# Optimization experiments

Measured on AMD Instinct MI355X. Metric: run time of the kernel, lower is better.

## Reference

```python
import jax, jax.numpy as jnp
import numpy as np
from math import sqrt

D_MODEL = 768
D_T = 256
N_HEADS = 12
HEAD_DIM = D_MODEL // N_HEADS
SCALE = sqrt(HEAD_DIM)


def setup_inputs() -> dict:
    key = jax.random.key(0)
    ks = jax.random.split(key, 11)
    b, l = 8, 1024
    inv = 1.0 / sqrt(D_MODEL)
    inv_t = 1.0 / sqrt(D_T)
    return {
        "x": jax.random.normal(ks[0], (b, l, D_MODEL), dtype=jnp.float32),
        "t": jax.random.normal(ks[1], (b, D_T), dtype=jnp.float32),
        "rel_pos_bias": jax.random.normal(ks[2], (N_HEADS, l, l), dtype=jnp.float32),
        # torch Linear weights: [out_features, in_features]
        "Wx_q": jax.random.normal(ks[3], (D_MODEL, D_MODEL), dtype=jnp.float32) * inv,
        "Wx_k": jax.random.normal(ks[4], (D_MODEL, D_MODEL), dtype=jnp.float32) * inv,
        "Wx_v": jax.random.normal(ks[5], (D_MODEL, D_MODEL), dtype=jnp.float32) * inv,
        "Wt_q": jax.random.normal(ks[6], (D_MODEL, D_T), dtype=jnp.float32) * inv_t,
        "Wt_k": jax.random.normal(ks[7], (D_MODEL, D_T), dtype=jnp.float32) * inv_t,
        "Wt_v": jax.random.normal(ks[8], (D_MODEL, D_T), dtype=jnp.float32) * inv_t,
        "W_o": jax.random.normal(ks[9], (D_MODEL, D_MODEL), dtype=jnp.float32) * inv,
        "b_o": jax.random.normal(ks[10], (D_MODEL,), dtype=jnp.float32) * 0.01,
    }


def _split_heads(y):
    # [b, l, n*d] -> [b, n, l, d]
    b, l, _ = y.shape
    return y.reshape(b, l, N_HEADS, HEAD_DIM).transpose(0, 2, 1, 3)


def reference(x, t, rel_pos_bias, Wx_q, Wx_k, Wx_v, Wt_q, Wt_k, Wt_v, W_o, b_o):
    # time-conditioned QKV: per-batch additive shift broadcast over seq
    q = _split_heads(x @ Wx_q.T + (t @ Wt_q.T)[:, None, :])
    k = _split_heads(x @ Wx_k.T + (t @ Wt_k.T)[:, None, :])
    v = _split_heads(x @ Wx_v.T + (t @ Wt_v.T)[:, None, :])
    attn = jnp.einsum("bnld,bnmd->bnlm", q, k) / SCALE
    attn = attn + rel_pos_bias  # [n,l,l] broadcasts over batch
    probs = jax.nn.softmax(attn, axis=-1)
    o = jnp.einsum("bnlm,bnmd->bnld", probs, v)
    b, _, l, _ = o.shape
    o = o.transpose(0, 2, 1, 3).reshape(b, l, D_MODEL)
    return o @ W_o.T + b_o
```

## Files before the change

### kernel.cpp

```cpp
#include <hip/hip_runtime.h>
#include <hip/hip_bf16.h>
#include <stdint.h>

typedef __bf16 bf16_t;
typedef __attribute__((ext_vector_type(8))) __bf16 bf16x8;
typedef __attribute__((ext_vector_type(4))) __bf16 bf16x4;
typedef __attribute__((ext_vector_type(4))) float f32x4;

#define DEVI __device__ __forceinline__

DEVI void gll16(const void* g, void* lds_base_wave_uniform) {
  __builtin_amdgcn_global_load_lds(
      (const __attribute__((address_space(1))) uint32_t*)(uintptr_t)g,
      (__attribute__((address_space(3))) uint32_t*)(uintptr_t)lds_base_wave_uniform,
      16, 0, 0);
}

__global__ void cvt_f32_to_bf16(const float* __restrict__ src, bf16_t* __restrict__ dst, int n) {
  int i = (blockIdx.x * blockDim.x + threadIdx.x) * 4;
  if (i >= n) return;
  float4 v = *(const float4*)(src + i);
  bf16x4 o = {(bf16_t)v.x, (bf16_t)v.y, (bf16_t)v.z, (bf16_t)v.w};
  *(bf16x4*)(dst + i) = o;
}

__global__ void shift_kernel(const float* __restrict__ t,
                             const float* __restrict__ wtq,
                             const float* __restrict__ wtk,
                             const float* __restrict__ wtv,
                             float* __restrict__ shift) {
  int idx = blockIdx.x * blockDim.x + threadIdx.x;
  if (idx >= 8 * 2304) return;
  int b = idx / 2304, n = idx % 2304;
  const float* w = (n < 768) ? (wtq + (size_t)n * 256)
                 : (n < 1536) ? (wtk + (size_t)(n - 768) * 256)
                              : (wtv + (size_t)(n - 1536) * 256);
  const float4* tv = (const float4*)(t + (size_t)b * 256);
  const float4* wv = (const float4*)w;
  float acc = 0.f;
#pragma unroll 8
  for (int i = 0; i < 64; i++) {
    float4 a = tv[i], c = wv[i];
    acc += a.x * c.x + a.y * c.y + a.z * c.z + a.w * c.w;
  }
  shift[idx] = acc;
}

template <int MODE>
__global__ __launch_bounds__(256, 2) void gemm_bt(
    const bf16_t* __restrict__ A, const bf16_t* __restrict__ B,
    const float* __restrict__ add, void* __restrict__ Cout,
    int M, int N, int K) {
  __shared__ alignas(16) bf16_t As[128 * 32];
  __shared__ alignas(16) bf16_t Bs[128 * 32];
  const int t = threadIdx.x, l = t & 63, w = t >> 6;
  const int wr = w >> 1, wc = w & 1;
  const int bm = blockIdx.x, bn = blockIdx.y;

  f32x4 acc[4][4] = {};

  const int srow = t >> 2;
  const int scol = (t & 3) * 8;
  const bf16_t* Ab = A + ((size_t)bm * 128 + srow) * K + scol;
  const bf16_t* Bb = B + ((size_t)bn * 128 + srow) * K + scol;
  char* AsB = (char*)As + w * 1024;
  char* BsB = (char*)Bs + w * 1024;
  const size_t K64 = (size_t)64 * K;

  const int ro = (l & 15) * 32 + (l >> 4) * 8;
  const bf16_t* ApA = As + (wr * 64) * 32 + ro;
  const bf16_t* BpB = Bs + (wc * 64) * 32 + ro;

  for (int k0 = 0; k0 < K; k0 += 32) {
    __syncthreads();
    gll16(Ab + k0, AsB);
    gll16(Ab + K64 + k0, AsB + 4096);
    gll16(Bb + k0, BsB);
    gll16(Bb + K64 + k0, BsB + 4096);
    __syncthreads();
    bf16x8 af[4], bfr[4];
#pragma unroll
    for (int i = 0; i < 4; i++) {
      af[i]  = *(const bf16x8*)(ApA + i * 16 * 32);
      bfr[i] = *(const bf16x8*)(BpB + i * 16 * 32);
    }
#pragma unroll
    for (int mi = 0; mi < 4; mi++)
#pragma unroll
      for (int ni = 0; ni < 4; ni++)
        acc[mi][ni] = __builtin_amdgcn_mfma_f32_16x16x32_bf16(af[mi], bfr[ni], acc[mi][ni], 0, 0, 0);
  }

  const int row0 = bm * 128 + wr * 64 + (l >> 4) * 4;
  const int col0 = bn * 128 + wc * 64 + (l & 15);
  if (MODE == 0) {
    bf16_t* C = (bf16_t*)Cout;
    const float* sh = add + (size_t)((bm * 128) >> 10) * N;
#pragma unroll
    for (int ni = 0; ni < 4; ni++) {
      const int col = col0 + ni * 16;
      const float s0 = sh[col];
#pragma unroll
      for (int mi = 0; mi < 4; mi++)
#pragma unroll
        for (int i = 0; i < 4; i++)
          C[(size_t)(row0 + mi * 16 + i) * N + col] = (bf16_t)(acc[mi][ni][i] + s0);
    }
  } else {
    float* C = (float*)Cout;
#pragma unroll
    for (int ni = 0; ni < 4; ni++) {
      const int col = col0 + ni * 16;
      const float s0 = add[col];
#pragma unroll
      for (int mi = 0; mi < 4; mi++)
#pragma unroll
        for (int i = 0; i < 4; i++)
          C[(size_t)(row0 + mi * 16 + i) * N + col] = acc[mi][ni][i] + s0;
    }
  }
}

__global__ __launch_bounds__(256, 2) void attn_fused(
    const bf16_t* __restrict__ qkv,
    const float* __restrict__ bias,
    bf16_t* __restrict__ o) {
  const int id = blockIdx.x;
  const int slot = id >> 3;
  const int qt = slot & 15;
  const int grp = (id & 7) + 8 * (slot >> 4);
  const int h = grp % 12, b = grp / 12;
  const int t = threadIdx.x, l = t & 63, w = t >> 6;

  __shared__ alignas(16) bf16_t Vt[64 * 64];
  __shared__ alignas(16) bf16_t Ps[4][16 * 64];

  const size_t rowb = (size_t)b * 1024;

  bf16x8 qf[2];
  {
    const bf16_t* qp = qkv + (rowb + qt * 64 + w * 16 + (l & 15)) * 2304 + h * 64 + (l >> 4) * 8;
    qf[0] = *(const bf16x8*)qp;
    qf[1] = *(const bf16x8*)(qp + 32);
  }

  const float* bbase = bias + ((size_t)h << 20)
                     + (size_t)(qt * 64 + w * 16 + (l >> 4) * 4) * 1024 + (l & 15);
  const bf16_t* kbase = qkv + rowb * 2304 + 768 + h * 64 + (l >> 4) * 8;

  float m_run[4] = {-INFINITY, -INFINITY, -INFINITY, -INFINITY};
  float l_run[4] = {0.f, 0.f, 0.f, 0.f};
  f32x4 oacc[4] = {};

  const float LOG2E = 1.44269504088896f;
  const float C1 = 0.125f * 1.44269504088896f;

  for (int kt = 0; kt < 16; kt++) {
    bf16x8 kf[4][2];
    {
      const bf16_t* kb = kbase + (size_t)(kt * 64) * 2304;
#pragma unroll
      for (int nf = 0; nf < 4; nf++) {
        const bf16_t* kr = kb + (size_t)(nf * 16 + (l & 15)) * 2304;
        kf[nf][0] = *(const bf16x8*)kr;
        kf[nf][1] = *(const bf16x8*)(kr + 32);
      }
    }
    float barr[4][4];
    {
      const float* bb = bbase + kt * 64;
#pragma unroll
      for (int i = 0; i < 4; i++)
#pragma unroll
        for (int nf = 0; nf < 4; nf++)
          barr[i][nf] = bb[(size_t)i * 1024 + nf * 16];
    }

    __syncthreads();
    {
      const bf16_t* vp = qkv + (rowb + kt * 64 + l) * 2304 + 1536 + h * 64 + w * 16;
      bf16x8 v0 = *(const bf16x8*)vp;
      bf16x8 v1 = *(const bf16x8*)(vp + 8);
#pragma unroll
      for (int j = 0; j < 16; j++) {
        const int d = w * 16 + j;
        const int addr = d * 64 + (((l >> 3) ^ (d & 7)) * 8) + (l & 7);
        Vt[addr] = (j < 8) ? v0[j] : v1[j - 8];
      }
    }

    f32x4 sv[4];
#pragma unroll
    for (int nf = 0; nf < 4; nf++) {
      f32x4 z = {0.f, 0.f, 0.f, 0.f};
      z = __builtin_amdgcn_mfma_f32_16x16x32_bf16(qf[0], kf[nf][0], z, 0, 0, 0);
      z = __builtin_amdgcn_mfma_f32_16x16x32_bf16(qf[1], kf[nf][1], z, 0, 0, 0);
      sv[nf] = z;
    }

    float p[4][4];
    float alpha[4];
#pragma unroll
    for (int i = 0; i < 4; i++) {
      float lg[4];
#pragma unroll
      for (int nf = 0; nf < 4; nf++)
        lg[nf] = fmaf(sv[nf][i], C1, barr[i][nf] * LOG2E);
      float mx = fmaxf(fmaxf(lg[0], lg[1]), fmaxf(lg[2], lg[3]));
      mx = fmaxf(mx, __shfl_xor(mx, 1));
      mx = fmaxf(mx, __shfl_xor(mx, 2));
      mx = fmaxf(mx, __shfl_xor(mx, 4));
      mx = fmaxf(mx, __shfl_xor(mx, 8));
      const float mnew = fmaxf(m_run[i], mx);
      alpha[i] = exp2f(m_run[i] - mnew);
      m_run[i] = mnew;
      float rs = 0.f;
#pragma unroll
      for (int nf = 0; nf < 4; nf++) {
        p[nf][i] = exp2f(lg[nf] - mnew);
        rs += p[nf][i];
      }
      rs += __shfl_xor(rs, 1);
      rs += __shfl_xor(rs, 2);
      rs += __shfl_xor(rs, 4);
      rs += __shfl_xor(rs, 8);
      l_run[i] = l_run[i] * alpha[i] + rs;
    }

    bf16_t* Pw = Ps[w];
#pragma unroll
    for (int nf = 0; nf < 4; nf++)
#pragma unroll
      for (int i = 0; i < 4; i++) {
        const int rq = (l >> 4) * 4 + i;
        const int kp = nf * 16 + (l & 15);
        Pw[rq * 64 + (((kp >> 3) ^ (rq & 7)) * 8) + (kp & 7)] = (bf16_t)p[nf][i];
      }
#pragma unroll
    for (int nf2 = 0; nf2 < 4; nf2++)
#pragma unroll
      for (int i = 0; i < 4; i++)
        oacc[nf2][i] *= alpha[i];

    __syncthreads();

    bf16x8 pf[2];
#pragma unroll
    for (int kc = 0; kc < 2; kc++) {
      const int rq = l & 15;
      const int chunk = kc * 4 + (l >> 4);
      pf[kc] = *(const bf16x8*)(Pw + rq * 64 + ((chunk ^ (rq & 7)) * 8));
    }
#pragma unroll
    for (int nf2 = 0; nf2 < 4; nf2++) {
      const int d = nf2 * 16 + (l & 15);
      const bf16_t* vb = Vt + d * 64;
      bf16x8 vf0 = *(const bf16x8*)(vb + (((l >> 4) ^ (d & 7)) * 8));
      bf16x8 vf1 = *(const bf16x8*)(vb + ((((l >> 4) + 4) ^ (d & 7)) * 8));
      oacc[nf2] = __builtin_amdgcn_mfma_f32_16x16x32_bf16(pf[0], vf0, oacc[nf2], 0, 0, 0);
      oacc[nf2] = __builtin_amdgcn_mfma_f32_16x16x32_bf16(pf[1], vf1, oacc[nf2], 0, 0, 0);
    }
  }

#pragma unroll
  for (int i = 0; i < 4; i++) {
    const float inv = 1.0f / l_run[i];
    const size_t row = rowb + qt * 64 + w * 16 + (l >> 4) * 4 + i;
#pragma unroll
    for (int nf2 = 0; nf2 < 4; nf2++)
      o[row * 768 + h * 64 + nf2 * 16 + (l & 15)] = (bf16_t)(oacc[nf2][i] * inv);
  }
}

extern "C" void kernel_launch(void* const* d_in, const int* in_sizes, int n_in,
                              void* d_out, int out_size, void* d_ws, size_t ws_size,
                              hipStream_t stream) {
  const float* x    = (const float*)d_in[0];
  const float* tin  = (const float*)d_in[1];
  const float* bias = (const float*)d_in[2];
  const float* Wxq  = (const float*)d_in[3];
  const float* Wxk  = (const float*)d_in[4];
  const float* Wxv  = (const float*)d_in[5];
  const float* Wtq  = (const float*)d_in[6];
  const float* Wtk  = (const float*)d_in[7];
  const float* Wtv  = (const float*)d_in[8];
  const float* Wo   = (const float*)d_in[9];
  const float* bo   = (const float*)d_in[10];
  float* out = (float*)d_out;

  char* ws = (char*)d_ws;
  bf16_t* x_bf    = (bf16_t*)(ws);
  bf16_t* wcat    = (bf16_t*)(ws + 12582912);
  bf16_t* wo_bf   = (bf16_t*)(ws + 16121856);
  float*  shift   = (float*) (ws + 17301504);
  bf16_t* qkvb    = (bf16_t*)(ws + 17375232);
  bf16_t* obuf    = (bf16_t*)(ws + 55123968);

  const int W = 768 * 768;
  cvt_f32_to_bf16<<<6144, 256, 0, stream>>>(x, x_bf, 8192 * 768);
  cvt_f32_to_bf16<<<576, 256, 0, stream>>>(Wxq, wcat, W);
  cvt_f32_to_bf16<<<576, 256, 0, stream>>>(Wxk, wcat + W, W);
  cvt_f32_to_bf16<<<576, 256, 0, stream>>>(Wxv, wcat + 2 * W, W);
  cvt_f32_to_bf16<<<576, 256, 0, stream>>>(Wo, wo_bf, W);
  shift_kernel<<<72, 256, 0, stream>>>(tin, Wtq, Wtk, Wtv, shift);
  gemm_bt<0><<<dim3(64, 18), 256, 0, stream>>>(x_bf, wcat, shift, qkvb, 8192, 2304, 768);
  attn_fused<<<1536, 256, 0, stream>>>(qkvb, bias, obuf);
  gemm_bt<1><<<dim3(64, 6), 256, 0, stream>>>(obuf, wo_bf, bo, out, 8192, 768, 768);
}
```

Measured before the change: 344.7 us.

## Transpose QK MFMA so each lane owns one query row; lazy softmax rescale

The S=QK^T MFMA operands are swapped, so each lane holds four consecutive key columns of a single query row. This allows vectorized float4 bias loads, a row max and row sum done with only two cross-lane shuffles, and packed bf16x4 stores of P to LDS. The online-softmax rescale is skipped unless some row max grows by more than 8 in log2 units, and launch bounds are raised to 4 blocks per CU. Global V loads are issued before the barrier and P is read back before the second barrier. The risks are register pressure under the tighter occupancy bound and possible exp2 overflow headroom from deferred rescaling, though the threshold keeps values bounded.

```diff
diff --git a/kernel.cpp b/kernel.cpp
--- a/kernel.cpp
+++ b/kernel.cpp
@@ -121,7 +121,7 @@
   }
 }
 
-__global__ __launch_bounds__(256, 2) void attn_fused(
+__global__ __launch_bounds__(256, 4) void attn_fused(
     const bf16_t* __restrict__ qkv,
     const float* __restrict__ bias,
     bf16_t* __restrict__ o) {
@@ -131,132 +131,132 @@
   const int grp = (id & 7) + 8 * (slot >> 4);
   const int h = grp % 12, b = grp / 12;
   const int t = threadIdx.x, l = t & 63, w = t >> 6;
+  const int s = l & 15, g = l >> 4;
 
   __shared__ alignas(16) bf16_t Vt[64 * 64];
   __shared__ alignas(16) bf16_t Ps[4][16 * 64];
 
   const size_t rowb = (size_t)b * 1024;
+  const int qrow = qt * 64 + w * 16 + s;
 
   bf16x8 qf[2];
   {
-    const bf16_t* qp = qkv + (rowb + qt * 64 + w * 16 + (l & 15)) * 2304 + h * 64 + (l >> 4) * 8;
+    const bf16_t* qp = qkv + (rowb + qrow) * 2304 + h * 64 + g * 8;
     qf[0] = *(const bf16x8*)qp;
     qf[1] = *(const bf16x8*)(qp + 32);
   }
 
-  const float* bbase = bias + ((size_t)h << 20)
-                     + (size_t)(qt * 64 + w * 16 + (l >> 4) * 4) * 1024 + (l & 15);
-  const bf16_t* kbase = qkv + rowb * 2304 + 768 + h * 64 + (l >> 4) * 8;
-
-  float m_run[4] = {-INFINITY, -INFINITY, -INFINITY, -INFINITY};
-  float l_run[4] = {0.f, 0.f, 0.f, 0.f};
+  const bf16_t* kbase = qkv + rowb * 2304 + 768 + h * 64 + g * 8;
+  const float*  bbase = bias + ((size_t)h << 20) + (size_t)qrow * 1024 + g * 4;
+
+  float m_run = -INFINITY, l_run = 0.f;
   f32x4 oacc[4] = {};
-
   const float LOG2E = 1.44269504088896f;
   const float C1 = 0.125f * 1.44269504088896f;
 
   for (int kt = 0; kt < 16; kt++) {
     bf16x8 kf[4][2];
     {
-      const bf16_t* kb = kbase + (size_t)(kt * 64) * 2304;
+      const bf16_t* kb = kbase + (size_t)(kt * 64 + s) * 2304;
 #pragma unroll
       for (int nf = 0; nf < 4; nf++) {
-        const bf16_t* kr = kb + (size_t)(nf * 16 + (l & 15)) * 2304;
+        const bf16_t* kr = kb + (size_t)(nf * 16) * 2304;
         kf[nf][0] = *(const bf16x8*)kr;
         kf[nf][1] = *(const bf16x8*)(kr + 32);
       }
     }
-    float barr[4][4];
+    f32x4 bv[4];
     {
       const float* bb = bbase + kt * 64;
 #pragma unroll
-      for (int i = 0; i < 4; i++)
-#pragma unroll
-        for (int nf = 0; nf < 4; nf++)
-          barr[i][nf] = bb[(size_t)i * 1024 + nf * 16];
-    }
-
-    __syncthreads();
+      for (int nf = 0; nf < 4; nf++)
+        bv[nf] = *(const f32x4*)(bb + nf * 16);
+    }
+    bf16x8 v0, v1;
     {
       const bf16_t* vp = qkv + (rowb + kt * 64 + l) * 2304 + 1536 + h * 64 + w * 16;
-      bf16x8 v0 = *(const bf16x8*)vp;
-      bf16x8 v1 = *(const bf16x8*)(vp + 8);
-#pragma unroll
-      for (int j = 0; j < 16; j++) {
-        const int d = w * 16 + j;
-        const int addr = d * 64 + (((l >> 3) ^ (d & 7)) * 8) + (l & 7);
-        Vt[addr] = (j < 8) ? v0[j] : v1[j - 8];
-      }
+      v0 = *(const bf16x8*)vp;
+      v1 = *(const bf16x8*)(vp + 8);
+    }
+
+    __syncthreads();
+#pragma unroll
+    for (int j = 0; j < 16; j++) {
+      const int d = w * 16 + j;
+      const int addr = d * 64 + (((l >> 3) ^ (d & 7)) * 8) + (l & 7);
+      Vt[addr] = (j < 8) ? v0[j] : v1[j - 8];
     }
 
     f32x4 sv[4];
 #pragma unroll
     for (int nf = 0; nf < 4; nf++) {
       f32x4 z = {0.f, 0.f, 0.f, 0.f};
-      z = __builtin_amdgcn_mfma_f32_16x16x32_bf16(qf[0], kf[nf][0], z, 0, 0, 0);
-      z = __builtin_amdgcn_mfma_f32_16x16x32_bf16(qf[1], kf[nf][1], z, 0, 0, 0);
+      z = __builtin_amdgcn_mfma_f32_16x16x32_bf16(kf[nf][0], qf[0], z, 0, 0, 0);
+      z = __builtin_amdgcn_mfma_f32_16x16x32_bf16(kf[nf][1], qf[1], z, 0, 0, 0);
       sv[nf] = z;
     }
 
-    float p[4][4];
-    float alpha[4];
-#pragma unroll
-    for (int i = 0; i < 4; i++) {
-      float lg[4];
-#pragma unroll
-      for (int nf = 0; nf < 4; nf++)
-        lg[nf] = fmaf(sv[nf][i], C1, barr[i][nf] * LOG2E);
-      float mx = fmaxf(fmaxf(lg[0], lg[1]), fmaxf(lg[2], lg[3]));
-      mx = fmaxf(mx, __shfl_xor(mx, 1));
-      mx = fmaxf(mx, __shfl_xor(mx, 2));
-      mx = fmaxf(mx, __shfl_xor(mx, 4));
-      mx = fmaxf(mx, __shfl_xor(mx, 8));
-      const float mnew = fmaxf(m_run[i], mx);
-      alpha[i] = exp2f(m_run[i] - mnew);
-      m_run[i] = mnew;
-      float rs = 0.f;
+    float lg[4][4];
+#pragma unroll
+    for (int nf = 0; nf < 4; nf++)
+#pragma unroll
+      for (int i = 0; i < 4; i++)
+        lg[nf][i] = fmaf(sv[nf][i], C1, bv[nf][i] * LOG2E);
+
+    float mx = fmaxf(fmaxf(fmaxf(lg[0][0], lg[0][1]), fmaxf(lg[0][2], lg[0][3])),
+                     fmaxf(fmaxf(lg[1][0], lg[1][1]), fmaxf(lg[1][2], lg[1][3])));
+    mx = fmaxf(mx, fmaxf(fmaxf(fmaxf(lg[2][0], lg[2][1]), fmaxf(lg[2][2], lg[2][3])),
+                         fmaxf(fmaxf(lg[3][0], lg[3][1]), fmaxf(lg[3][2], lg[3][3]))));
+    mx = fmaxf(mx, __shfl_xor(mx, 16));
+    mx = fmaxf(mx, __shfl_xor(mx, 32));
+
+    if (!__all(mx - m_run <= 8.0f)) {
+      const float mnew = fmaxf(m_run, mx);
+      const float alpha = exp2f(m_run - mnew);
+      m_run = mnew;
+      l_run *= alpha;
+#pragma unroll
+      for (int i = 0; i < 4; i++) {
+        const float a_pv = __shfl(alpha, g * 4 + i);
+#pragma unroll
+        for (int nf2 = 0; nf2 < 4; nf2++) oacc[nf2][i] *= a_pv;
+      }
+    }
+
+    float rs = 0.f;
+#pragma unroll
+    for (int nf = 0; nf < 4; nf++)
+#pragma unroll
+      for (int i = 0; i < 4; i++) {
+        lg[nf][i] = exp2f(lg[nf][i] - m_run);
+        rs += lg[nf][i];
+      }
+    rs += __shfl_xor(rs, 16);
+    rs += __shfl_xor(rs, 32);
+    l_run += rs;
+
+    bf16_t* Pw = Ps[w];
+    {
+      char* pb = (char*)Pw + s * 128 + (g & 1) * 8;
 #pragma unroll
       for (int nf = 0; nf < 4; nf++) {
-        p[nf][i] = exp2f(lg[nf] - mnew);
-        rs += p[nf][i];
+        bf16x4 pk = {(bf16_t)lg[nf][0], (bf16_t)lg[nf][1], (bf16_t)lg[nf][2], (bf16_t)lg[nf][3]};
+        *(bf16x4*)(pb + ((2 * nf + (g >> 1)) ^ (s & 7)) * 16) = pk;
       }
-      rs += __shfl_xor(rs, 1);
-      rs += __shfl_xor(rs, 2);
-      rs += __shfl_xor(rs, 4);
-      rs += __shfl_xor(rs, 8);
-      l_run[i] = l_run[i] * alpha[i] + rs;
-    }
-
-    bf16_t* Pw = Ps[w];
-#pragma unroll
-    for (int nf = 0; nf < 4; nf++)
-#pragma unroll
-      for (int i = 0; i < 4; i++) {
-        const int rq = (l >> 4) * 4 + i;
-        const int kp = nf * 16 + (l & 15);
-        Pw[rq * 64 + (((kp >> 3) ^ (rq & 7)) * 8) + (kp & 7)] = (bf16_t)p[nf][i];
-      }
-#pragma unroll
-    for (int nf2 = 0; nf2 < 4; nf2++)
-#pragma unroll
-      for (int i = 0; i < 4; i++)
-        oacc[nf2][i] *= alpha[i];
+    }
+    bf16x8 pf[2];
+#pragma unroll
+    for (int c = 0; c < 2; c++)
+      pf[c] = *(const bf16x8*)((char*)Pw + s * 128 + ((4 * c + g) ^ (s & 7)) * 16);
 
     __syncthreads();
 
-    bf16x8 pf[2];
-#pragma unroll
-    for (int kc = 0; kc < 2; kc++) {
-      const int rq = l & 15;
-      const int chunk = kc * 4 + (l >> 4);
-      pf[kc] = *(const bf16x8*)(Pw + rq * 64 + ((chunk ^ (rq & 7)) * 8));
-    }
 #pragma unroll
     for (int nf2 = 0; nf2 < 4; nf2++) {
-      const int d = nf2 * 16 + (l & 15);
+      const int d = nf2 * 16 + s;
       const bf16_t* vb = Vt + d * 64;
-      bf16x8 vf0 = *(const bf16x8*)(vb + (((l >> 4) ^ (d & 7)) * 8));
-      bf16x8 vf1 = *(const bf16x8*)(vb + ((((l >> 4) + 4) ^ (d & 7)) * 8));
+      bf16x8 vf0 = *(const bf16x8*)(vb + ((g ^ (d & 7)) * 8));
+      bf16x8 vf1 = *(const bf16x8*)(vb + (((g + 4) ^ (d & 7)) * 8));
       oacc[nf2] = __builtin_amdgcn_mfma_f32_16x16x32_bf16(pf[0], vf0, oacc[nf2], 0, 0, 0);
       oacc[nf2] = __builtin_amdgcn_mfma_f32_16x16x32_bf16(pf[1], vf1, oacc[nf2], 0, 0, 0);
     }
@@ -264,11 +264,11 @@
 
 #pragma unroll
   for (int i = 0; i < 4; i++) {
-    const float inv = 1.0f / l_run[i];
-    const size_t row = rowb + qt * 64 + w * 16 + (l >> 4) * 4 + i;
+    const float inv = 1.0f / __shfl(l_run, g * 4 + i);
+    const size_t row = rowb + qt * 64 + w * 16 + g * 4 + i;
 #pragma unroll
     for (int nf2 = 0; nf2 < 4; nf2++)
-      o[row * 768 + h * 64 + nf2 * 16 + (l & 15)] = (bf16_t)(oacc[nf2][i] * inv);
+      o[row * 768 + h * 64 + nf2 * 16 + s] = (bf16_t)(oacc[nf2][i] * inv);
   }
 }
 
```

New measurement: 374.8 us. 1.09x slower.
